# Performance work log

Measured on AMD Instinct MI355X. Metric: run time of the kernel, lower is better.

Reference implementation:

```python
import jax, jax.numpy as jnp
import numpy as np

HIDDEN = 1024
HEADS = 16
HEAD_DIM = HIDDEN // HEADS  # 64
B, S = 2, 2048


def setup_inputs() -> dict:
    key = jax.random.key(0)
    ks = jax.random.split(key, 8)
    scale = 1.0 / np.sqrt(HIDDEN)
    return {
        "hidden_states": jax.random.normal(ks[0], (B, S, HIDDEN), dtype=jnp.float32),
        "head_mask": jnp.ones((1, HEADS, 1, 1), dtype=jnp.float32),
        "Wq": jax.random.normal(ks[1], (HIDDEN, HIDDEN), dtype=jnp.float32) * scale,
        "bq": jnp.zeros((HIDDEN,), dtype=jnp.float32),
        "Wk": jax.random.normal(ks[2], (HIDDEN, HIDDEN), dtype=jnp.float32) * scale,
        "bk": jnp.zeros((HIDDEN,), dtype=jnp.float32),
        "Wv": jax.random.normal(ks[3], (HIDDEN, HIDDEN), dtype=jnp.float32) * scale,
        "bv": jnp.zeros((HIDDEN,), dtype=jnp.float32),
    }


def _split_heads(x):
    # [B, S, HIDDEN] -> [B, HEADS, S, HEAD_DIM]
    b, s, _ = x.shape
    return x.reshape(b, s, HEADS, HEAD_DIM).transpose(0, 2, 1, 3)


def reference(hidden_states, head_mask, Wq, bq, Wk, bk, Wv, bv):
    q = _split_heads(hidden_states @ Wq + bq)
    k = _split_heads(hidden_states @ Wk + bk)
    v = _split_heads(hidden_states @ Wv + bv)
    # [B, H, S, S] attention scores (eager, full matrix as in original)
    scores = jnp.einsum("bhqd,bhkd->bhqk", q, k) / jnp.sqrt(jnp.float32(HEAD_DIM))
    probs = jax.nn.softmax(scores, axis=-1)
    probs = probs * head_mask  # post-softmax multiplicative head mask
    ctx = jnp.einsum("bhqk,bhkd->bhqd", probs, v)
    b, h, s, d = ctx.shape
    return ctx.transpose(0, 2, 1, 3).reshape(b, s, h * d)
```

## Files before the change

kernel.cpp:

```cpp
#include <hip/hip_runtime.h>
#include <hip/hip_bf16.h>
#include <stdint.h>

#define B_  2
#define S_  2048
#define H_  16
#define D_  64
#define HID 1024

typedef __bf16 bf16x8 __attribute__((ext_vector_type(8)));
typedef float  f32x4  __attribute__((ext_vector_type(4)));
typedef float  f32x16 __attribute__((ext_vector_type(16)));
typedef unsigned int u32x4 __attribute__((ext_vector_type(4)));
typedef unsigned short ush;

__device__ __forceinline__ ush f2bf(float f) {
    __bf16 b = (__bf16)f;
    return __builtin_bit_cast(ush, b);
}
__device__ __forceinline__ unsigned pk2(float a, float b) {
    return (unsigned)f2bf(a) | ((unsigned)f2bf(b) << 16);
}
__device__ __forceinline__ float xchg32f(float x) {
    return __shfl_xor(x, 32, 64);
}
__device__ __forceinline__ float exp2fast(float x) {
#if __has_builtin(__builtin_amdgcn_exp2f)
    return __builtin_amdgcn_exp2f(x);
#else
    float r; asm("v_exp_f32 %0, %1" : "=v"(r) : "v"(x)); return r;
#endif
}
__device__ __forceinline__ void gld16(const void* g, void* l) {
    __builtin_amdgcn_global_load_lds(
        (const __attribute__((address_space(1))) unsigned*)g,
        (__attribute__((address_space(3))) unsigned*)l, 16, 0, 0);
}

__global__ __launch_bounds__(256) void cvt_hid(const float* __restrict__ in,
                                               ush* __restrict__ outp) {
    size_t base = ((size_t)blockIdx.x * 256 + threadIdx.x) * 16;
    #pragma unroll
    for (int half = 0; half < 2; ++half) {
        float4 v0 = *reinterpret_cast<const float4*>(in + base + half * 8);
        float4 v1 = *reinterpret_cast<const float4*>(in + base + half * 8 + 4);
        u32x4 o = { pk2(v0.x, v0.y), pk2(v0.z, v0.w),
                    pk2(v1.x, v1.y), pk2(v1.z, v1.w) };
        *reinterpret_cast<u32x4*>(outp + base + half * 8) = o;
    }
}

__global__ __launch_bounds__(256) void wtrans(
    const float* __restrict__ Wq, const float* __restrict__ Wk,
    const float* __restrict__ Wv, ush* __restrict__ wt)
{
    const int tid = threadIdx.x;
    const int k0 = blockIdx.x * 64, n0 = blockIdx.y * 64, sel = blockIdx.z;
    const float* W = sel == 0 ? Wq : (sel == 1 ? Wk : Wv);
    ush* o = wt + (size_t)sel * HID * HID;
    __shared__ ush lT[64][72];
    #pragma unroll
    for (int i = 0; i < 4; ++i) {
        int c = tid + i * 256;
        int kr = c >> 4, c4 = (c & 15) << 2;
        float4 v = *reinterpret_cast<const float4*>(W + (size_t)(k0 + kr) * HID + n0 + c4);
        lT[kr][c4 + 0] = f2bf(v.x); lT[kr][c4 + 1] = f2bf(v.y);
        lT[kr][c4 + 2] = f2bf(v.z); lT[kr][c4 + 3] = f2bf(v.w);
    }
    __syncthreads();
    #pragma unroll
    for (int i = 0; i < 2; ++i) {
        int c = tid + i * 256;
        int nr = c >> 3, k8 = (c & 7) << 3;
        ush t[8];
        #pragma unroll
        for (int u = 0; u < 8; ++u) t[u] = lT[k8 + u][nr];
        u32x4 ov = { (unsigned)t[0] | ((unsigned)t[1] << 16),
                     (unsigned)t[2] | ((unsigned)t[3] << 16),
                     (unsigned)t[4] | ((unsigned)t[5] << 16),
                     (unsigned)t[6] | ((unsigned)t[7] << 16) };
        *reinterpret_cast<u32x4*>(o + (size_t)(n0 + nr) * HID + k0 + k8) = ov;
    }
}

__global__ __launch_bounds__(256) void proj(
    const ush* __restrict__ hidb, const ush* __restrict__ wt,
    const float* __restrict__ bq, const float* __restrict__ bk,
    const float* __restrict__ bv,
    ush* __restrict__ qd, ush* __restrict__ kd, ush* __restrict__ vtd)
{
    const int tid = threadIdx.x;
    const int wave = tid >> 6, lane = tid & 63;
    const int fr = lane & 15, fq = lane >> 4;
    const int wr = wave >> 1, wc = wave & 1;
    const int m0 = blockIdx.x * 128;
    const int n0 = blockIdx.y * 128;
    const int wsel = n0 >> 10;

    __shared__ char pool[65536];

    const int cr = lane >> 3;
    const int cs = lane & 7;

    f32x4 acc[4][4] = {};

    const ush* Asrc = hidb + (size_t)m0 * HID;
    const ush* Bsrc = wt + (size_t)n0 * HID;

    auto stage = [&](int buf, int kk) {
        #pragma unroll
        for (int j = 0; j < 4; ++j) {
            int ch = wave * 4 + j;
            int r = ch * 8 + cr;
            int so = kk + ((cs ^ (r & 7)) << 3);
            gld16(Asrc + (size_t)r * HID + so, pool + buf * 16384 + ch * 1024);
            gld16(Bsrc + (size_t)r * HID + so, pool + 32768 + buf * 16384 + ch * 1024);
        }
    };

    stage(0, 0);
    __syncthreads();
    int buf = 0;
    for (int ks = 0; ks < 16; ++ks) {
        if (ks < 15) stage(buf ^ 1, (ks + 1) * 64);
        const char* ab = pool + buf * 16384;
        const char* bb = pool + 32768 + buf * 16384;
        #pragma unroll
        for (int c = 0; c < 2; ++c) {
            bf16x8 a[4], b[4];
            #pragma unroll
            for (int i = 0; i < 4; ++i) {
                int ra = wr * 64 + i * 16 + fr;
                a[i] = *reinterpret_cast<const bf16x8*>(
                    ab + ((ra * 128 + c * 64 + fq * 16) ^ ((ra & 7) << 4)));
                int rb = wc * 64 + i * 16 + fr;
                b[i] = *reinterpret_cast<const bf16x8*>(
                    bb + ((rb * 128 + c * 64 + fq * 16) ^ ((rb & 7) << 4)));
            }
            __builtin_amdgcn_s_setprio(1);
            #pragma unroll
            for (int i = 0; i < 4; ++i)
                #pragma unroll
                for (int j = 0; j < 4; ++j)
                    acc[i][j] = __builtin_amdgcn_mfma_f32_16x16x32_bf16(
                        a[i], b[j], acc[i][j], 0, 0, 0);
            __builtin_amdgcn_s_setprio(0);
        }
        __syncthreads();
        buf ^= 1;
    }

    const int bi = m0 >> 11;
    const int s0 = m0 & 2047;
    const float* bias = wsel == 0 ? bq : (wsel == 1 ? bk : bv);
    const int nb = n0 & 1023;

    if (wsel < 2) {
        ush* dst = wsel == 0 ? qd : kd;
        const float scale = wsel == 0 ? 0.18033688011112042f : 1.0f;
        #pragma unroll
        for (int j = 0; j < 4; ++j) {
            int n = nb + wc * 64 + j * 16 + fr;
            int hh = n >> 6, d = n & 63;
            float bb2 = bias[n];
            const size_t rowb = (size_t)(bi * H_ + hh) * S_;
            #pragma unroll
            for (int i = 0; i < 4; ++i)
                #pragma unroll
                for (int e = 0; e < 4; ++e) {
                    int s = s0 + wr * 64 + i * 16 + fq * 4 + e;
                    dst[(rowb + s) * D_ + d] = f2bf((acc[i][j][e] + bb2) * scale);
                }
        }
    } else {
        ush (*lT)[136] = (ush (*)[136])pool;
        #pragma unroll
        for (int j = 0; j < 4; ++j) {
            int nl = wc * 64 + j * 16 + fr;
            float bb2 = bias[nb + nl];
            #pragma unroll
            for (int i = 0; i < 4; ++i)
                #pragma unroll
                for (int e = 0; e < 4; ++e)
                    lT[wr * 64 + i * 16 + fq * 4 + e][nl] = f2bf(acc[i][j][e] + bb2);
        }
        __syncthreads();
        #pragma unroll
        for (int c2 = 0; c2 < 8; ++c2) {
            int cid = tid + c2 * 256;
            int nl = cid >> 4, s8 = (cid & 15) * 8;
            int n = nb + nl, hh = n >> 6, d = n & 63;
            ush t[8];
            #pragma unroll
            for (int u = 0; u < 8; ++u) t[u] = lT[s8 + u][nl];
            u32x4 ov = { (unsigned)t[0] | ((unsigned)t[1] << 16),
                         (unsigned)t[2] | ((unsigned)t[3] << 16),
                         (unsigned)t[4] | ((unsigned)t[5] << 16),
                         (unsigned)t[6] | ((unsigned)t[7] << 16) };
            *reinterpret_cast<u32x4*>(
                vtd + ((size_t)(bi * H_ + hh) * D_ + d) * S_ + s0 + s8) = ov;
        }
    }
}

#define PVSTEP(ps, ksc) do {                                                   \
    constexpr int rb_ = ((ksc) & 1) * 8;                                       \
    u32x4 pw_ = { pk2(ps[rb_ + 0], ps[rb_ + 1]), pk2(ps[rb_ + 2], ps[rb_ + 3]),\
                  pk2(ps[rb_ + 4], ps[rb_ + 5]), pk2(ps[rb_ + 6], ps[rb_ + 7])};\
    bf16x8 pf_ = __builtin_bit_cast(bf16x8, pw_);                              \
    const int vb0_ = l31 * 128 + (ksc) * 32 + hi * 16;                         \
    bf16x8 v0_ = *reinterpret_cast<const bf16x8*>(vb + (vb0_ ^ swz));          \
    bf16x8 v1_ = *reinterpret_cast<const bf16x8*>(vb + ((vb0_ + 4096) ^ swz)); \
    accoA = __builtin_amdgcn_mfma_f32_32x32x16_bf16(v0_, pf_, accoA, 0, 0, 0); \
    accoB = __builtin_amdgcn_mfma_f32_32x32x16_bf16(v1_, pf_, accoB, 0, 0, 0); \
} while (0)

__global__ __launch_bounds__(512) void attn(
    const ush* __restrict__ qg, const ush* __restrict__ kg,
    const ush* __restrict__ vtg, const float* __restrict__ hm,
    float* __restrict__ out)
{
    const int tid = threadIdx.x;
    const int wave = tid >> 6, lane = tid & 63;
    const int l31 = lane & 31, hi = lane >> 5;
    const int swz = (l31 & 7) << 4;
    const int qt = blockIdx.x, h = blockIdx.y, bi = blockIdx.z;
    const size_t ho = (size_t)(bi * H_ + h) * S_ * D_;
    const ush* Q  = qg + ho;
    const ush* K  = kg + ho;
    const ush* VT = vtg + ho;

    __shared__ ush lK[2][64][64];
    __shared__ ush lV[2][64][64];

    const int q = qt * 256 + wave * 32 + l31;
    bf16x8 qf[4];
    #pragma unroll
    for (int ks = 0; ks < 4; ++ks)
        qf[ks] = *reinterpret_cast<const bf16x8*>(Q + (size_t)q * D_ + ks * 16 + hi * 8);

    f32x16 accoA = {}, accoB = {};
    float mi = -1e30f, li = 0.f;

    const int dr = wave * 8 + (lane >> 3);
    const int kr = (dr & ~12) | ((dr & 4) << 1) | ((dr & 8) >> 1);
    const int ss = ((lane & 7) ^ (lane >> 3)) * 8;

    gld16(K + (size_t)kr * D_ + ss, &lK[0][wave * 8][0]);
    gld16(VT + (size_t)dr * S_ + ss, &lV[0][wave * 8][0]);
    __syncthreads();

    int buf = 0;
    for (int t = 0; t < 32; ++t) {
        if (t < 31) {
            int kv0 = (t + 1) * 64;
            gld16(K + (size_t)(kv0 + kr) * D_ + ss, &lK[buf ^ 1][wave * 8][0]);
            gld16(VT + (size_t)dr * S_ + kv0 + ss, &lV[buf ^ 1][wave * 8][0]);
        }
        const char* kb = (const char*)&lK[buf][0][0];
        const char* vb = (const char*)&lV[buf][0][0];

        f32x16 p0 = {}, p1 = {};
        #pragma unroll
        for (int ks = 0; ks < 4; ++ks) {
            int kb0 = l31 * 128 + ks * 32 + hi * 16;
            bf16x8 k0 = *reinterpret_cast<const bf16x8*>(kb + (kb0 ^ swz));
            bf16x8 k1 = *reinterpret_cast<const bf16x8*>(kb + ((kb0 + 4096) ^ swz));
            __builtin_amdgcn_s_setprio(1);
            p0 = __builtin_amdgcn_mfma_f32_32x32x16_bf16(k0, qf[ks], p0, 0, 0, 0);
            p1 = __builtin_amdgcn_mfma_f32_32x32x16_bf16(k1, qf[ks], p1, 0, 0, 0);
            __builtin_amdgcn_s_setprio(0);
        }

        float pm0 = fmaxf(p0[0], p1[0]), pm1 = fmaxf(p0[1], p1[1]);
        float pm2 = fmaxf(p0[2], p1[2]), pm3 = fmaxf(p0[3], p1[3]);
        #pragma unroll
        for (int r = 4; r < 16; r += 4) {
            pm0 = fmaxf(pm0, fmaxf(p0[r],     p1[r]));
            pm1 = fmaxf(pm1, fmaxf(p0[r + 1], p1[r + 1]));
            pm2 = fmaxf(pm2, fmaxf(p0[r + 2], p1[r + 2]));
            pm3 = fmaxf(pm3, fmaxf(p0[r + 3], p1[r + 3]));
        }
        float pm = fmaxf(fmaxf(pm0, pm1), fmaxf(pm2, pm3));
        pm = fmaxf(pm, xchg32f(pm));

        const bool defer = __all(pm - mi <= 8.0f);
        const float mn = defer ? mi : fmaxf(mi, pm);
        float rs0 = 0.f, rs1 = 0.f, rs2 = 0.f, rs3 = 0.f;
        #pragma unroll
        for (int r = 0; r < 16; r += 4) {
            p0[r]     = exp2fast(p0[r]     - mn); rs0 += p0[r];
            p0[r + 1] = exp2fast(p0[r + 1] - mn); rs1 += p0[r + 1];
            p0[r + 2] = exp2fast(p0[r + 2] - mn); rs2 += p0[r + 2];
            p0[r + 3] = exp2fast(p0[r + 3] - mn); rs3 += p0[r + 3];
            p1[r]     = exp2fast(p1[r]     - mn); rs0 += p1[r];
            p1[r + 1] = exp2fast(p1[r + 1] - mn); rs1 += p1[r + 1];
            p1[r + 2] = exp2fast(p1[r + 2] - mn); rs2 += p1[r + 2];
            p1[r + 3] = exp2fast(p1[r + 3] - mn); rs3 += p1[r + 3];
        }
        float rs = (rs0 + rs1) + (rs2 + rs3);
        rs += xchg32f(rs);
        if (defer) {
            li += rs;
        } else {
            const float sc = exp2fast(mi - mn);
            li = li * sc + rs;
            mi = mn;
            #pragma unroll
            for (int r = 0; r < 16; ++r) { accoA[r] *= sc; accoB[r] *= sc; }
        }

        __builtin_amdgcn_s_setprio(1);
        PVSTEP(p0, 0);
        PVSTEP(p0, 1);
        PVSTEP(p1, 2);
        PVSTEP(p1, 3);
        __builtin_amdgcn_s_setprio(0);

        __syncthreads();
        buf ^= 1;
    }

    const float inv = hm[h] / li;
    float* orow = out + ((size_t)bi * S_ + q) * HID + h * D_;
    #pragma unroll
    for (int g = 0; g < 4; ++g) {
        f32x4 oA, oB;
        #pragma unroll
        for (int e = 0; e < 4; ++e) {
            oA[e] = accoA[g * 4 + e] * inv;
            oB[e] = accoB[g * 4 + e] * inv;
        }
        *reinterpret_cast<f32x4*>(orow + g * 8 + hi * 4) = oA;
        *reinterpret_cast<f32x4*>(orow + 32 + g * 8 + hi * 4) = oB;
    }
}

extern "C" void kernel_launch(void* const* d_in, const int* in_sizes, int n_in,
                              void* d_out, int out_size, void* d_ws, size_t ws_size,
                              hipStream_t stream) {
    const float* hid = (const float*)d_in[0];
    const float* hm  = (const float*)d_in[1];
    const float* Wq  = (const float*)d_in[2];
    const float* bq  = (const float*)d_in[3];
    const float* Wk  = (const float*)d_in[4];
    const float* bk  = (const float*)d_in[5];
    const float* Wv  = (const float*)d_in[6];
    const float* bv  = (const float*)d_in[7];
    float* out = (float*)d_out;

    const size_t NE = (size_t)B_ * H_ * S_ * D_;
    ush* qws  = (ush*)d_ws;
    ush* kws  = qws + NE;
    ush* vt   = kws + NE;
    ush* hidb = (ush*)d_out;
    ush* wt   = hidb + NE;

    cvt_hid<<<1024, 256, 0, stream>>>(hid, hidb);
    wtrans<<<dim3(16, 16, 3), 256, 0, stream>>>(Wq, Wk, Wv, wt);
    proj<<<dim3(32, 24), 256, 0, stream>>>(hidb, wt, bq, bk, bv, qws, kws, vt);
    attn<<<dim3(8, 16, 2), 512, 0, stream>>>(qws, kws, vt, hm, out);
}
```

Before: 107.5 us.

## Triple-buffer attention K/V with software-pipelined QK and remap block grids

The attention loop becomes a software pipeline over three LDS buffers. While softmax and PV run on the current tile, the QK^T MFMAs for the next tile are issued and a load two tiles ahead is in flight, with explicit vmcnt waits and raw barriers replacing __syncthreads. The projection and attention grids are flattened to 1D with a remapped block order, likely to change L2 locality and CU placement. The cost is extra LDS per block and hand-written waitcnt and barrier logic that has to stay correct.

```diff
diff --git a/kernel.cpp b/kernel.cpp
--- a/kernel.cpp
+++ b/kernel.cpp
@@ -93,8 +93,9 @@
     const int wave = tid >> 6, lane = tid & 63;
     const int fr = lane & 15, fq = lane >> 4;
     const int wr = wave >> 1, wc = wave & 1;
-    const int m0 = blockIdx.x * 128;
-    const int n0 = blockIdx.y * 128;
+    const int L = blockIdx.x;
+    const int m0 = (L / 24) * 128;
+    const int n0 = (L % 24) * 128;
     const int wsel = n0 >> 10;
 
     __shared__ char pool[65536];
@@ -215,6 +216,85 @@
     accoB = __builtin_amdgcn_mfma_f32_32x32x16_bf16(v1_, pf_, accoB, 0, 0, 0); \
 } while (0)
 
+#define GLD(bf, kv0) do {                                                      \
+    gld16(K + (size_t)((kv0) + kr) * D_ + ss, &lK[bf][wave * 8][0]);           \
+    gld16(VT + (size_t)dr * S_ + (kv0) + ss, &lV[bf][wave * 8][0]);            \
+} while (0)
+
+#define WAITV2() asm volatile("s_waitcnt vmcnt(2)" ::: "memory")
+#define WAITV0() asm volatile("s_waitcnt vmcnt(0)" ::: "memory")
+#define BARRIER() do { __builtin_amdgcn_s_barrier();                           \
+                       __builtin_amdgcn_sched_barrier(0); } while (0)
+
+#define QKS(bf) do {                                                           \
+    const char* kb = (const char*)&lK[bf][0][0];                               \
+    p0 = f32x16{}; p1 = f32x16{};                                              \
+    _Pragma("unroll")                                                          \
+    for (int ks = 0; ks < 4; ++ks) {                                           \
+        int kb0 = l31 * 128 + ks * 32 + hi * 16;                               \
+        bf16x8 k0 = *reinterpret_cast<const bf16x8*>(kb + (kb0 ^ swz));        \
+        bf16x8 k1 = *reinterpret_cast<const bf16x8*>(kb + ((kb0 + 4096) ^ swz));\
+        __builtin_amdgcn_s_setprio(1);                                         \
+        p0 = __builtin_amdgcn_mfma_f32_32x32x16_bf16(k0, qf[ks], p0, 0, 0, 0); \
+        p1 = __builtin_amdgcn_mfma_f32_32x32x16_bf16(k1, qf[ks], p1, 0, 0, 0); \
+        __builtin_amdgcn_s_setprio(0);                                         \
+    }                                                                          \
+} while (0)
+
+#define SMAX() do {                                                            \
+    float pm0 = fmaxf(p0[0], p1[0]), pm1 = fmaxf(p0[1], p1[1]);                \
+    float pm2 = fmaxf(p0[2], p1[2]), pm3 = fmaxf(p0[3], p1[3]);                \
+    _Pragma("unroll")                                                          \
+    for (int r = 4; r < 16; r += 4) {                                          \
+        pm0 = fmaxf(pm0, fmaxf(p0[r],     p1[r]));                             \
+        pm1 = fmaxf(pm1, fmaxf(p0[r + 1], p1[r + 1]));                         \
+        pm2 = fmaxf(pm2, fmaxf(p0[r + 2], p1[r + 2]));                         \
+        pm3 = fmaxf(pm3, fmaxf(p0[r + 3], p1[r + 3]));                         \
+    }                                                                          \
+    float pm = fmaxf(fmaxf(pm0, pm1), fmaxf(pm2, pm3));                        \
+    pm = fmaxf(pm, xchg32f(pm));                                               \
+    const bool defer = __all(pm - mi <= 8.0f);           \
+    const float mn = defer ? mi : fmaxf(mi, pm);                               \
+    float rs0 = 0.f, rs1 = 0.f, rs2 = 0.f, rs3 = 0.f;                          \
+    _Pragma("unroll")                                                          \
+    for (int r = 0; r < 16; r += 4) {                                          \
+        p0[r]     = exp2fast(p0[r]     - mn); rs0 += p0[r];                    \
+        p0[r + 1] = exp2fast(p0[r + 1] - mn); rs1 += p0[r + 1];                \
+        p0[r + 2] = exp2fast(p0[r + 2] - mn); rs2 += p0[r + 2];                \
+        p0[r + 3] = exp2fast(p0[r + 3] - mn); rs3 += p0[r + 3];                \
+        p1[r]     = exp2fast(p1[r]     - mn); rs0 += p1[r];                    \
+        p1[r + 1] = exp2fast(p1[r + 1] - mn); rs1 += p1[r + 1];                \
+        p1[r + 2] = exp2fast(p1[r + 2] - mn); rs2 += p1[r + 2];                \
+        p1[r + 3] = exp2fast(p1[r + 3] - mn); rs3 += p1[r + 3];                \
+    }                                                                          \
+    float rs = (rs0 + rs1) + (rs2 + rs3);                                      \
+    rs += xchg32f(rs);                                                         \
+    if (defer) {                                                               \
+        li += rs;                                                              \
+    } else {                                                                   \
+        const float sc = exp2fast(mi - mn);                                    \
+        li = li * sc + rs;                                                     \
+        mi = mn;                                                               \
+        _Pragma("unroll")                                                      \
+        for (int r = 0; r < 16; ++r) { accoA[r] *= sc; accoB[r] *= sc; }       \
+    }                                                                          \
+} while (0)
+
+#define PVALL(bf) do {                                                         \
+    const char* vb = (const char*)&lV[bf][0][0];                               \
+    __builtin_amdgcn_s_setprio(1);                                             \
+    PVSTEP(p0, 0); PVSTEP(p0, 1); PVSTEP(p1, 2); PVSTEP(p1, 3);                \
+    __builtin_amdgcn_s_setprio(0);                                             \
+} while (0)
+
+#define FSTEP(t, bc, bn, bf2) do {                                             \
+    GLD(bf2, ((t) + 2) * 64);                                                  \
+    SMAX();                                                                    \
+    PVALL(bc);                                                                 \
+    WAITV2(); BARRIER();                                                       \
+    QKS(bn);                                                                   \
+} while (0)
+
 __global__ __launch_bounds__(512) void attn(
     const ush* __restrict__ qg, const ush* __restrict__ kg,
     const ush* __restrict__ vtg, const float* __restrict__ hm,
@@ -224,14 +304,15 @@
     const int wave = tid >> 6, lane = tid & 63;
     const int l31 = lane & 31, hi = lane >> 5;
     const int swz = (l31 & 7) << 4;
-    const int qt = blockIdx.x, h = blockIdx.y, bi = blockIdx.z;
+    const int g = blockIdx.x & 31, qt = blockIdx.x >> 5;
+    const int h = g >> 1, bi = g & 1;
     const size_t ho = (size_t)(bi * H_ + h) * S_ * D_;
     const ush* Q  = qg + ho;
     const ush* K  = kg + ho;
     const ush* VT = vtg + ho;
 
-    __shared__ ush lK[2][64][64];
-    __shared__ ush lV[2][64][64];
+    __shared__ ush lK[3][64][64];
+    __shared__ ush lV[3][64][64];
 
     const int q = qt * 256 + wave * 32 + l31;
     bf16x8 qf[4];
@@ -240,99 +321,42 @@
         qf[ks] = *reinterpret_cast<const bf16x8*>(Q + (size_t)q * D_ + ks * 16 + hi * 8);
 
     f32x16 accoA = {}, accoB = {};
+    f32x16 p0, p1;
     float mi = -1e30f, li = 0.f;
 
     const int dr = wave * 8 + (lane >> 3);
     const int kr = (dr & ~12) | ((dr & 4) << 1) | ((dr & 8) >> 1);
     const int ss = ((lane & 7) ^ (lane >> 3)) * 8;
 
-    gld16(K + (size_t)kr * D_ + ss, &lK[0][wave * 8][0]);
-    gld16(VT + (size_t)dr * S_ + ss, &lV[0][wave * 8][0]);
-    __syncthreads();
-
-    int buf = 0;
-    for (int t = 0; t < 32; ++t) {
-        if (t < 31) {
-            int kv0 = (t + 1) * 64;
-            gld16(K + (size_t)(kv0 + kr) * D_ + ss, &lK[buf ^ 1][wave * 8][0]);
-            gld16(VT + (size_t)dr * S_ + kv0 + ss, &lV[buf ^ 1][wave * 8][0]);
-        }
-        const char* kb = (const char*)&lK[buf][0][0];
-        const char* vb = (const char*)&lV[buf][0][0];
-
-        f32x16 p0 = {}, p1 = {};
-        #pragma unroll
-        for (int ks = 0; ks < 4; ++ks) {
-            int kb0 = l31 * 128 + ks * 32 + hi * 16;
-            bf16x8 k0 = *reinterpret_cast<const bf16x8*>(kb + (kb0 ^ swz));
-            bf16x8 k1 = *reinterpret_cast<const bf16x8*>(kb + ((kb0 + 4096) ^ swz));
-            __builtin_amdgcn_s_setprio(1);
-            p0 = __builtin_amdgcn_mfma_f32_32x32x16_bf16(k0, qf[ks], p0, 0, 0, 0);
-            p1 = __builtin_amdgcn_mfma_f32_32x32x16_bf16(k1, qf[ks], p1, 0, 0, 0);
-            __builtin_amdgcn_s_setprio(0);
-        }
-
-        float pm0 = fmaxf(p0[0], p1[0]), pm1 = fmaxf(p0[1], p1[1]);
-        float pm2 = fmaxf(p0[2], p1[2]), pm3 = fmaxf(p0[3], p1[3]);
-        #pragma unroll
-        for (int r = 4; r < 16; r += 4) {
-            pm0 = fmaxf(pm0, fmaxf(p0[r],     p1[r]));
-            pm1 = fmaxf(pm1, fmaxf(p0[r + 1], p1[r + 1]));
-            pm2 = fmaxf(pm2, fmaxf(p0[r + 2], p1[r + 2]));
-            pm3 = fmaxf(pm3, fmaxf(p0[r + 3], p1[r + 3]));
-        }
-        float pm = fmaxf(fmaxf(pm0, pm1), fmaxf(pm2, pm3));
-        pm = fmaxf(pm, xchg32f(pm));
-
-        const bool defer = __all(pm - mi <= 8.0f);
-        const float mn = defer ? mi : fmaxf(mi, pm);
-        float rs0 = 0.f, rs1 = 0.f, rs2 = 0.f, rs3 = 0.f;
-        #pragma unroll
-        for (int r = 0; r < 16; r += 4) {
-            p0[r]     = exp2fast(p0[r]     - mn); rs0 += p0[r];
-            p0[r + 1] = exp2fast(p0[r + 1] - mn); rs1 += p0[r + 1];
-            p0[r + 2] = exp2fast(p0[r + 2] - mn); rs2 += p0[r + 2];
-            p0[r + 3] = exp2fast(p0[r + 3] - mn); rs3 += p0[r + 3];
-            p1[r]     = exp2fast(p1[r]     - mn); rs0 += p1[r];
-            p1[r + 1] = exp2fast(p1[r + 1] - mn); rs1 += p1[r + 1];
-            p1[r + 2] = exp2fast(p1[r + 2] - mn); rs2 += p1[r + 2];
-            p1[r + 3] = exp2fast(p1[r + 3] - mn); rs3 += p1[r + 3];
-        }
-        float rs = (rs0 + rs1) + (rs2 + rs3);
-        rs += xchg32f(rs);
-        if (defer) {
-            li += rs;
-        } else {
-            const float sc = exp2fast(mi - mn);
-            li = li * sc + rs;
-            mi = mn;
-            #pragma unroll
-            for (int r = 0; r < 16; ++r) { accoA[r] *= sc; accoB[r] *= sc; }
-        }
-
-        __builtin_amdgcn_s_setprio(1);
-        PVSTEP(p0, 0);
-        PVSTEP(p0, 1);
-        PVSTEP(p1, 2);
-        PVSTEP(p1, 3);
-        __builtin_amdgcn_s_setprio(0);
-
-        __syncthreads();
-        buf ^= 1;
-    }
+    GLD(0, 0);
+    GLD(1, 64);
+    WAITV2(); BARRIER();
+    QKS(0);
+
+    for (int tt = 0; tt < 30; tt += 3) {
+        FSTEP(tt + 0, 0, 1, 2);
+        FSTEP(tt + 1, 1, 2, 0);
+        FSTEP(tt + 2, 2, 0, 1);
+    }
+    SMAX();
+    PVALL(0);
+    WAITV0(); BARRIER();
+    QKS(1);
+    SMAX();
+    PVALL(1);
 
     const float inv = hm[h] / li;
     float* orow = out + ((size_t)bi * S_ + q) * HID + h * D_;
     #pragma unroll
-    for (int g = 0; g < 4; ++g) {
+    for (int gg = 0; gg < 4; ++gg) {
         f32x4 oA, oB;
         #pragma unroll
         for (int e = 0; e < 4; ++e) {
-            oA[e] = accoA[g * 4 + e] * inv;
-            oB[e] = accoB[g * 4 + e] * inv;
-        }
-        *reinterpret_cast<f32x4*>(orow + g * 8 + hi * 4) = oA;
-        *reinterpret_cast<f32x4*>(orow + 32 + g * 8 + hi * 4) = oB;
+            oA[e] = accoA[gg * 4 + e] * inv;
+            oB[e] = accoB[gg * 4 + e] * inv;
+        }
+        *reinterpret_cast<f32x4*>(orow + gg * 8 + hi * 4) = oA;
+        *reinterpret_cast<f32x4*>(orow + 32 + gg * 8 + hi * 4) = oB;
     }
 }
 
@@ -358,6 +382,6 @@
 
     cvt_hid<<<1024, 256, 0, stream>>>(hid, hidb);
     wtrans<<<dim3(16, 16, 3), 256, 0, stream>>>(Wq, Wk, Wv, wt);
-    proj<<<dim3(32, 24), 256, 0, stream>>>(hidb, wt, bq, bk, bv, qws, kws, vt);
-    attn<<<dim3(8, 16, 2), 512, 0, stream>>>(qws, kws, vt, hm, out);
-}
+    proj<<<768, 256, 0, stream>>>(hidb, wt, bq, bk, bv, qws, kws, vt);
+    attn<<<256, 512, 0, stream>>>(qws, kws, vt, hm, out);
+}
```

Measured after the change: 103.8 us. 3.4% less time.
